# Kernel tuning notes

Hardware: AMD Instinct MI355X
Metric: run time of the kernel (lower is better)

The kernel has to match this reference:

```python
import jax, jax.numpy as jnp
import numpy as np

DIM = 1024
HEADS = 16
DHEAD = 64
INNER = HEADS * DHEAD
B, N = 1, 2048
ROPE_BASE = 10000.0
LN_EPS = 1e-5


def rope_tables(seq_len, d, dtype):
    # theta_i = 1 / base^(2i/d); emb = cat(freqs, freqs) -> cos/sin [N, d]
    theta = 1.0 / (ROPE_BASE ** (jnp.arange(0, d, 2, dtype=dtype) / d))
    pos = jnp.arange(seq_len, dtype=dtype)
    freqs = pos[:, None] * theta[None, :]          # [N, d/2]
    emb = jnp.concatenate([freqs, freqs], axis=-1)  # [N, d]
    return jnp.cos(emb), jnp.sin(emb)


def apply_rotary(x, cos, sin):
    # x: [B,H,N,D], cos/sin: [N,D]; interleaved rotation as in the torch code
    x1, x2 = x[..., ::2], x[..., 1::2]
    x_rot = jnp.stack([-x2, x1], axis=-1).reshape(x.shape)
    return x * cos + x_rot * sin


def setup_inputs() -> dict:
    key = jax.random.key(0)
    ks = jax.random.split(key, 6)
    x = jax.random.normal(ks[0], (B, N, DIM), dtype=jnp.float32)
    gamma = jnp.ones((DIM,), dtype=jnp.float32)
    Wq = jax.random.normal(ks[1], (DIM, INNER), dtype=jnp.float32) * 0.02
    Wkv = jax.random.normal(ks[2], (DIM, 2 * INNER), dtype=jnp.float32) * 0.02
    # near-identity per-head bilinear transform (torch inits toward identity)
    W_bilinear = jnp.eye(DHEAD, dtype=jnp.float32)[None] + \
        jax.random.normal(ks[3], (HEADS, DHEAD, DHEAD), dtype=jnp.float32) * 0.02
    Wo = jax.random.normal(ks[4], (INNER, DIM), dtype=jnp.float32) * 0.02
    return {"x": x, "gamma": gamma, "Wq": Wq, "Wkv": Wkv,
            "W_bilinear": W_bilinear, "Wo": Wo}


def reference(x, gamma, Wq, Wkv, W_bilinear, Wo):
    b, n, _ = x.shape
    # LayerNorm (beta = 0 buffer)
    mu = jnp.mean(x, axis=-1, keepdims=True)
    var = jnp.var(x, axis=-1, keepdims=True)
    xn = (x - mu) / jnp.sqrt(var + LN_EPS) * gamma

    q = xn @ Wq                                    # [B,N,INNER]
    kv = xn @ Wkv                                  # [B,N,2*INNER]
    k, v = jnp.split(kv, 2, axis=-1)

    def to_heads(t):
        return t.reshape(b, n, HEADS, DHEAD).transpose(0, 2, 1, 3)  # [B,H,N,D]

    q, k, v = map(to_heads, (q, k, v))

    cos, sin = rope_tables(n, DHEAD, x.dtype)
    q = apply_rotary(q, cos, sin) * (DHEAD ** -0.5)
    k = apply_rotary(k, cos, sin)

    # per-head bilinear transform of K
    kt = jnp.einsum('bhnd,hde->bhne', k, W_bilinear)
    sim = jnp.einsum('bhid,bhjd->bhij', q, kt)      # [B,H,N,N]
    attn = jax.nn.softmax(sim, axis=-1)
    out = jnp.einsum('bhij,bhjd->bhid', attn, v)    # [B,H,N,D]
    out = out.transpose(0, 2, 1, 3).reshape(b, n, INNER)
    return out @ Wo
```

## Files before the change

### kernel.cpp

```cpp
#include <hip/hip_runtime.h>
#include <hip/hip_bf16.h>


typedef unsigned short u16;
typedef __attribute__((ext_vector_type(4))) float f32x4;
typedef __attribute__((ext_vector_type(8))) __bf16 bf16x8;

struct alignas(8) US4 { u16 x, y, z, w; };

__device__ __forceinline__ u16 f2bf(float f) {
  union { float f; unsigned u; } v; v.f = f;
  unsigned r = v.u + 0x7FFFu + ((v.u >> 16) & 1u);
  return (u16)(r >> 16);
}
__device__ __forceinline__ unsigned pk2bf(float a, float b) {
  float2 f; f.x = a; f.y = b;
  __hip_bfloat162 h = __float22bfloat162_rn(f);
  union { __hip_bfloat162 h; unsigned u; } v; v.h = h;
  return v.u;
}

typedef void GVOID __attribute__((address_space(1)));
typedef void LVOID __attribute__((address_space(3)));

#if defined(__has_builtin)
#if __has_builtin(__builtin_amdgcn_global_load_lds)
#define HAS_GLD_LDS 1
#endif
#endif

__device__ __forceinline__ void gld16(const void* g, void* l) {
#ifdef HAS_GLD_LDS
  __builtin_amdgcn_global_load_lds((GVOID*)(void*)g, (LVOID*)l, 16, 0, 0);
#else
  struct alignas(16) U4 { unsigned a, b, c, d; };
  *(U4*)l = *(const U4*)g;
#endif
}

__device__ __forceinline__ f32x4 MFMA(bf16x8 a, bf16x8 b, f32x4 c) {
  return __builtin_amdgcn_mfma_f32_16x16x32_bf16(a, b, c, 0, 0, 0);
}

__device__ __forceinline__ int swz(int r, int q) {
  return r * 32 + ((q ^ ((r >> 1) & 3)) << 3);
}
__device__ __forceinline__ int swz_src_colb(int o) {
  const int r = o >> 6;
  return ((((o >> 4) & 3) ^ ((r >> 1) & 3)) << 4);
}
__device__ __forceinline__ int mswz4(int ee, int c) {
  return ee * 64 + ((c ^ (ee & 15)) << 2);
}
__device__ __forceinline__ int mswz1(int ee, int q) {
  return ee * 64 + ((((q >> 2) ^ (ee & 15)) << 2) | (q & 3));
}

__global__ __launch_bounds__(256) void prep_kernel(
    const float* __restrict__ x, const float* __restrict__ gamma,
    const float* __restrict__ Wq, const float* __restrict__ Wkv,
    const float* __restrict__ Wo, const float* __restrict__ Wb,
    u16* __restrict__ xn, u16* __restrict__ wqkvT, u16* __restrict__ woT,
    u16* __restrict__ wbT) {
  __shared__ __align__(16) float smem[64 * 65];
  const int bid = blockIdx.x, t = threadIdx.x;
  if (bid < 1040) {
    const float* src; u16* dst; int C, R, bx, by;
    if (bid < 256)      { src = Wq;  dst = wqkvT; R = 1024; C = 1024; bx = bid & 15; by = bid >> 4; }
    else if (bid < 768) { int i = bid - 256; src = Wkv; dst = wqkvT + 1024 * 1024; R = 1024; C = 2048; bx = i & 31; by = i >> 5; }
    else if (bid < 1024){ int i = bid - 768; src = Wo;  dst = woT; R = 1024; C = 1024; bx = i & 15; by = i >> 4; }
    else { int h = bid - 1024; src = Wb + (size_t)h * 4096; dst = wbT + (size_t)h * 4096; R = 64; C = 64; bx = 0; by = 0; }
    float (*tile)[65] = (float(*)[65])smem;
    const int c0 = bx * 64, r0 = by * 64;
    const int tx = t & 63, ty = t >> 6;
#pragma unroll
    for (int i = 0; i < 16; i++)
      tile[ty + i * 4][tx] = src[(size_t)(r0 + ty + i * 4) * C + c0 + tx];
    __syncthreads();
#pragma unroll
    for (int i = 0; i < 16; i++)
      dst[(size_t)(c0 + ty + i * 4) * R + r0 + tx] = f2bf(tile[tx][ty + i * 4]);
  } else {
    const int n = bid - 1040;
    const int w = t >> 6, lane = t & 63;
    const float4 v = *(const float4*)&x[(size_t)n * 1024 + t * 4];
    float s = v.x + v.y + v.z + v.w;
    float q = v.x * v.x + v.y * v.y + v.z * v.z + v.w * v.w;
#pragma unroll
    for (int off = 32; off; off >>= 1) {
      s += __shfl_down(s, off);
      q += __shfl_down(q, off);
    }
    if (lane == 0) { smem[w] = s; smem[4 + w] = q; }
    __syncthreads();
    s = smem[0] + smem[1] + smem[2] + smem[3];
    q = smem[4] + smem[5] + smem[6] + smem[7];
    const float mean = s * (1.0f / 1024.0f);
    const float var = q * (1.0f / 1024.0f) - mean * mean;
    const float inv = rsqrtf(var + 1e-5f);
    const float4 g = *(const float4*)&gamma[t * 4];
    US4 o;
    o.x = f2bf((v.x - mean) * inv * g.x);
    o.y = f2bf((v.y - mean) * inv * g.y);
    o.z = f2bf((v.z - mean) * inv * g.z);
    o.w = f2bf((v.w - mean) * inv * g.w);
    *(US4*)&xn[(size_t)n * 1024 + t * 4] = o;
  }
}

__global__ __launch_bounds__(256, 2) void gemm_qkv(
    const u16* __restrict__ A, const u16* __restrict__ B,
    const u16* __restrict__ wbT, u16* __restrict__ qh,
    u16* __restrict__ kth, u16* __restrict__ vt) {
  __shared__ u16 As[2 * 128 * 32];
  __shared__ u16 Bs[2 * 128 * 32];
  __shared__ u16 krs[2 * 8192];
  const int K = 1024;
  const int t = threadIdx.x;
  const int w = t >> 6, lane = t & 63, quad = lane >> 4, cc = lane & 15;
  const int bm = blockIdx.y << 7, bn = blockIdx.x << 7;
  const int wm = (w >> 1) << 6, wn = (w & 1) << 6;
  const f32x4 fzero = {0.f, 0.f, 0.f, 0.f};
  f32x4 acc[4][4];
#pragma unroll
  for (int i = 0; i < 4; i++)
#pragma unroll
    for (int j = 0; j < 4; j++) acc[i][j] = fzero;

  const char* gA = (const char*)A;
  const char* gB = (const char*)B;
  for (int k0 = 0; k0 < K; k0 += 64) {
    __syncthreads();
#pragma unroll
    for (int i = 0; i < 4; i++) {
      const int o = (i * 256 + t) * 16;
      const int sub = o >> 13, row = (o >> 6) & 127, colb = swz_src_colb(o);
      gld16(gA + (((size_t)(bm + row) * K + k0 + sub * 32) << 1) + colb, (char*)As + o);
      gld16(gB + (((size_t)(bn + row) * K + k0 + sub * 32) << 1) + colb, (char*)Bs + o);
    }
    __syncthreads();
#pragma unroll
    for (int ks = 0; ks < 2; ks++) {
      bf16x8 af[4], bfr[4];
#pragma unroll
      for (int mi = 0; mi < 4; mi++)
        af[mi] = *(const bf16x8*)&As[ks * 4096 + swz(wm + mi * 16 + cc, quad)];
#pragma unroll
      for (int ni = 0; ni < 4; ni++)
        bfr[ni] = *(const bf16x8*)&Bs[ks * 4096 + swz(wn + ni * 16 + cc, quad)];
#pragma unroll
      for (int mi = 0; mi < 4; mi++)
#pragma unroll
        for (int ni = 0; ni < 4; ni++)
          acc[mi][ni] = MFMA(af[mi], bfr[ni], acc[mi][ni]);
    }
  }

  const int region = blockIdx.x >> 3;
  if (region == 0) {
#pragma unroll
    for (int ni = 0; ni < 4; ni++) {
      const int col = bn + wn + ni * 16 + cc;
      const int h = (col >> 6) & 15, d = col & 63;
      const float theta = __expf(-(float)(col & 31) * 0.2878231366242557f);
      const float sgn = (col & 1) ? 1.0f : -1.0f;
#pragma unroll
      for (int mi = 0; mi < 4; mi++) {
        const int row0 = bm + wm + mi * 16 + quad * 4;
#pragma unroll
        for (int r = 0; r < 4; r++) {
          const float val = acc[mi][ni][r];
          const float pr = __shfl_xor(val, 1);
          float sv, cv;
          __sincosf(theta * (float)(row0 + r), &sv, &cv);
          qh[((size_t)h * 2048 + row0 + r) * 64 + d] =
              f2bf((val * cv + sgn * pr * sv) * 0.125f);
        }
      }
    }
  } else if (region == 2) {
#pragma unroll
    for (int ni = 0; ni < 4; ni++) {
      const int col = bn + wn + ni * 16 + cc;
      const int h = (col >> 6) & 15, d = col & 63;
      u16* base = vt + ((size_t)h * 64 + d) * 2048;
#pragma unroll
      for (int mi = 0; mi < 4; mi++) {
        const int row0 = bm + wm + mi * 16 + quad * 4;
        uint2 pk;
        pk.x = pk2bf(acc[mi][ni][0], acc[mi][ni][1]);
        pk.y = pk2bf(acc[mi][ni][2], acc[mi][ni][3]);
        *(uint2*)&base[row0] = pk;
      }
    }
  } else {
    const int h2 = w & 1;
    u16* krh = krs + h2 * 8192;
#pragma unroll
    for (int ni = 0; ni < 4; ni++) {
      const int dloc = ni * 16 + cc;
      const int dsub = dloc >> 5;
      const int chunk = (dloc & 31) >> 3, elem = dloc & 7;
      const int col = bn + wn + ni * 16 + cc;
      const float theta = __expf(-(float)(col & 31) * 0.2878231366242557f);
      const float sgn = (col & 1) ? 1.0f : -1.0f;
#pragma unroll
      for (int mi = 0; mi < 4; mi++) {
        const int lrow0 = wm + mi * 16 + quad * 4;
#pragma unroll
        for (int r = 0; r < 4; r++) {
          const float val = acc[mi][ni][r];
          const float pr = __shfl_xor(val, 1);
          float sv, cv;
          __sincosf(theta * (float)(bm + lrow0 + r), &sv, &cv);
          const int row = lrow0 + r;
          krh[dsub * 4096 + row * 32 + ((chunk ^ ((row >> 1) & 3)) << 3) + elem] =
              f2bf(val * cv + sgn * pr * sv);
        }
      }
    }
    __syncthreads();
    const int hg0 = (bn >> 6) & 15;
#pragma unroll
    for (int i = 0; i < 2; i++) {
      const int o = (i * 256 + t) * 16;
      const int row = o >> 6;
      const int dsub = row >> 6, e = row & 63;
      const int colb = swz_src_colb(o);
      gld16((const char*)wbT + (((size_t)hg0 * 4096 + e * 64 + dsub * 32) << 1) + colb,
            (char*)As + o);
      gld16((const char*)wbT + (((size_t)(hg0 + 1) * 4096 + e * 64 + dsub * 32) << 1) + colb,
            (char*)Bs + o);
    }
    __syncthreads();
    const int wmrow = (w >> 1) << 6;
    const u16* Bsel = h2 ? Bs : As;
    f32x4 acc2[4][4];
#pragma unroll
    for (int i = 0; i < 4; i++)
#pragma unroll
      for (int j = 0; j < 4; j++) acc2[i][j] = fzero;
#pragma unroll
    for (int dsub = 0; dsub < 2; dsub++) {
      bf16x8 bfr[4];
#pragma unroll
      for (int et = 0; et < 4; et++)
        bfr[et] = *(const bf16x8*)&Bsel[swz(dsub * 64 + et * 16 + cc, quad)];
#pragma unroll
      for (int mi = 0; mi < 4; mi++) {
        const bf16x8 af = *(const bf16x8*)&krh[dsub * 4096 + swz(wmrow + mi * 16 + cc, quad)];
#pragma unroll
        for (int et = 0; et < 4; et++)
          acc2[mi][et] = MFMA(af, bfr[et], acc2[mi][et]);
      }
    }
    u16* Ck = kth + (size_t)(hg0 + h2) * 2048 * 64;
#pragma unroll
    for (int mi = 0; mi < 4; mi++) {
      const int n0 = bm + wmrow + mi * 16 + quad * 4;
#pragma unroll
      for (int et = 0; et < 4; et++) {
        const int e = et * 16 + cc;
#pragma unroll
        for (int r = 0; r < 4; r++)
          Ck[(size_t)(n0 + r) * 64 + e] = f2bf(acc2[mi][et][r]);
      }
    }
  }
}

__global__ __launch_bounds__(256, 2) void attn_kernel(
    const u16* __restrict__ qh, const u16* __restrict__ kth,
    const u16* __restrict__ vt, u16* __restrict__ aout) {
  __shared__ u16 Ks[2 * 128 * 32];
  __shared__ u16 Vs[4 * 64 * 32];
  __shared__ u16 Ps[4 * 64 * 32];
  const int t = threadIdx.x;
  const int w = t >> 6, lane = t & 63, quad = lane >> 4, cc = lane & 15;
  const int bid = blockIdx.x;
  const int h = (bid & 7) + ((bid >> 8) << 3);
  const int q0 = ((bid >> 3) & 31) << 6;
  const size_t hq = (size_t)h * (2048 * 64);
  const f32x4 fzero = {0.f, 0.f, 0.f, 0.f};
  const int g4 = (cc >> 1) & 3;

  bf16x8 ones;
  {
    union { u16 u; __bf16 b; } one; one.u = 0x3F80;
#pragma unroll
    for (int i = 0; i < 8; i++) ones[i] = one.b;
  }

#pragma unroll
  for (int i = 0; i < 2; i++) {
    const int o = (i * 256 + t) * 16;
    const int sub = o >> 12, row = (o >> 6) & 63, colb = swz_src_colb(o);
    gld16((const char*)qh + ((hq + (size_t)(q0 + row) * 64 + sub * 32) << 1) + colb,
          (char*)Ks + o);
  }
  __syncthreads();
  bf16x8 qf[4][2];
#pragma unroll
  for (int qn = 0; qn < 4; qn++)
#pragma unroll
    for (int ds = 0; ds < 2; ds++)
      qf[qn][ds] = *(const bf16x8*)&Ks[swz(ds * 64 + qn * 16 + cc, quad)];

  f32x4 oacc[4][4];
  f32x4 lacc[4];
#pragma unroll
  for (int mi = 0; mi < 4; mi++) {
    lacc[mi] = fzero;
#pragma unroll
    for (int et = 0; et < 4; et++) oacc[mi][et] = fzero;
  }

  u16* const psw = Ps + (w << 11);

  for (int jt = 0; jt < 16; jt++) {
    const int j0 = jt << 7;
    __syncthreads();
#pragma unroll
    for (int i = 0; i < 4; i++) {
      const int o = (i * 256 + t) * 16;
      const int colb = swz_src_colb(o);
      const int sub = o >> 13, row = (o >> 6) & 127;
      gld16((const char*)kth + ((hq + (size_t)(j0 + row) * 64 + sub * 32) << 1) + colb,
            (char*)Ks + o);
      const int vsub = o >> 12, vrow = (o >> 6) & 63;
      gld16((const char*)vt + ((hq + (size_t)vrow * 2048 + j0 + vsub * 32) << 1) + colb,
            (char*)Vs + o);
    }
    __syncthreads();

#pragma unroll
    for (int jm = 0; jm < 2; jm++) {
      const bf16x8 kf0 = *(const bf16x8*)&Ks[swz(w * 32 + jm * 16 + cc, quad)];
      const bf16x8 kf1 = *(const bf16x8*)&Ks[swz(128 + w * 32 + jm * 16 + cc, quad)];
      const int c16 = ((jm << 1) + (quad >> 1)) ^ g4;
      const int coff = (c16 << 3) + ((quad & 1) << 2);
#pragma unroll
      for (int qn = 0; qn < 4; qn++) {
        f32x4 s = MFMA(kf0, qf[qn][0], fzero);
        s = MFMA(kf1, qf[qn][1], s);
        uint2 pk;
        pk.x = pk2bf(__expf(s[0]), __expf(s[1]));
        pk.y = pk2bf(__expf(s[2]), __expf(s[3]));
        *(uint2*)&psw[((qn * 16 + cc) << 5) + coff] = pk;
      }
    }

    bf16x8 vf[4];
#pragma unroll
    for (int et = 0; et < 4; et++)
      vf[et] = *(const bf16x8*)&Vs[swz(w * 64 + et * 16 + cc, quad)];
#pragma unroll
    for (int mi = 0; mi < 4; mi++) {
      const bf16x8 pa = *(const bf16x8*)&psw[swz(mi * 16 + cc, quad)];
      lacc[mi] = MFMA(pa, ones, lacc[mi]);
#pragma unroll
      for (int et = 0; et < 4; et++) oacc[mi][et] = MFMA(pa, vf[et], oacc[mi][et]);
    }
  }

  float* OA = (float*)Ks;
  float* OB = (float*)Vs;
  float* lP = (float*)Ps;
  __syncthreads();
  if (w >= 2) {
    float* dst = (w == 2) ? OA : OB;
#pragma unroll
    for (int mi = 0; mi < 4; mi++) {
#pragma unroll
      for (int et = 0; et < 4; et++) {
        const int ee = et * 16 + cc;
        *(f32x4*)&dst[mswz4(ee, mi * 4 + quad)] = oacc[mi][et];
      }
      if (cc == 0)
#pragma unroll
        for (int r = 0; r < 4; r++)
          lP[64 * w + mi * 16 + quad * 4 + r] = lacc[mi][r];
    }
  }
  __syncthreads();
  if (w < 2) {
    const float* src = (w == 0) ? OA : OB;
    const float* lsrc = &lP[64 * (w + 2)];
#pragma unroll
    for (int mi = 0; mi < 4; mi++) {
#pragma unroll
      for (int et = 0; et < 4; et++) {
        const int ee = et * 16 + cc;
        oacc[mi][et] += *(const f32x4*)&src[mswz4(ee, mi * 4 + quad)];
      }
#pragma unroll
      for (int r = 0; r < 4; r++)
        lacc[mi][r] += lsrc[mi * 16 + quad * 4 + r];
    }
  }
  __syncthreads();
  if (w < 2) {
    float* dst = (w == 0) ? OA : OB;
#pragma unroll
    for (int mi = 0; mi < 4; mi++) {
#pragma unroll
      for (int et = 0; et < 4; et++) {
        const int ee = et * 16 + cc;
        *(f32x4*)&dst[mswz4(ee, mi * 4 + quad)] = oacc[mi][et];
      }
      if (cc == 0)
#pragma unroll
        for (int r = 0; r < 4; r++)
          lP[64 * w + mi * 16 + quad * 4 + r] = lacc[mi][r];
    }
  }
  __syncthreads();
  {
    const int q = lane;
    const float linv = 1.0f / (lP[q] + lP[64 + q]);
    unsigned obuf[8];
#pragma unroll
    for (int e = 0; e < 8; e++) {
      const int e0 = w * 16 + e * 2, e1 = e0 + 1;
      obuf[e] = pk2bf((OA[mswz1(e0, q)] + OB[mswz1(e0, q)]) * linv,
                      (OA[mswz1(e1, q)] + OB[mswz1(e1, q)]) * linv);
    }
    uint4* dst = (uint4*)&aout[(size_t)(q0 + q) * 1024 + h * 64 + w * 16];
    dst[0] = *(uint4*)&obuf[0];
    dst[1] = *(uint4*)&obuf[4];
  }
}

__global__ __launch_bounds__(256, 2) void gemm64_bt_f32(
    const u16* __restrict__ A, const u16* __restrict__ B, float* __restrict__ C,
    int M, int N, int K) {
  __shared__ u16 As[2 * 64 * 32];
  __shared__ u16 Bs[2 * 64 * 32];
  const int t = threadIdx.x;
  const int w = t >> 6, lane = t & 63, quad = lane >> 4, cc = lane & 15;
  const int bm = blockIdx.y << 6, bn = blockIdx.x << 6;
  const int wm = (w >> 1) << 5, wn = (w & 1) << 5;
  const f32x4 fzero = {0.f, 0.f, 0.f, 0.f};
  f32x4 acc[2][2];
#pragma unroll
  for (int i = 0; i < 2; i++)
#pragma unroll
    for (int j = 0; j < 2; j++) acc[i][j] = fzero;

  const char* gA = (const char*)A;
  const char* gB = (const char*)B;
  for (int k0 = 0; k0 < K; k0 += 64) {
    __syncthreads();
#pragma unroll
    for (int i = 0; i < 2; i++) {
      const int o = (i * 256 + t) * 16;
      const int sub = o >> 12, row = (o >> 6) & 63, colb = swz_src_colb(o);
      gld16(gA + (((size_t)(bm + row) * K + k0 + sub * 32) << 1) + colb, (char*)As + o);
      gld16(gB + (((size_t)(bn + row) * K + k0 + sub * 32) << 1) + colb, (char*)Bs + o);
    }
    __syncthreads();
#pragma unroll
    for (int ks = 0; ks < 2; ks++) {
      bf16x8 af[2], bfr[2];
#pragma unroll
      for (int mi = 0; mi < 2; mi++)
        af[mi] = *(const bf16x8*)&As[ks * 2048 + swz(wm + mi * 16 + cc, quad)];
#pragma unroll
      for (int ni = 0; ni < 2; ni++)
        bfr[ni] = *(const bf16x8*)&Bs[ks * 2048 + swz(wn + ni * 16 + cc, quad)];
#pragma unroll
      for (int mi = 0; mi < 2; mi++)
#pragma unroll
        for (int ni = 0; ni < 2; ni++)
          acc[mi][ni] = MFMA(af[mi], bfr[ni], acc[mi][ni]);
    }
  }
#pragma unroll
  for (int mi = 0; mi < 2; mi++) {
    const int row = bm + wm + mi * 16 + quad * 4;
#pragma unroll
    for (int ni = 0; ni < 2; ni++) {
      const int col = bn + wn + ni * 16 + cc;
#pragma unroll
      for (int r = 0; r < 4; r++) C[(size_t)(row + r) * N + col] = acc[mi][ni][r];
    }
  }
}

extern "C" void kernel_launch(void* const* d_in, const int* in_sizes, int n_in,
                              void* d_out, int out_size, void* d_ws, size_t ws_size,
                              hipStream_t stream) {
  (void)in_sizes; (void)n_in; (void)out_size; (void)ws_size;
  const float* x     = (const float*)d_in[0];
  const float* gamma = (const float*)d_in[1];
  const float* Wq    = (const float*)d_in[2];
  const float* Wkv   = (const float*)d_in[3];
  const float* Wb    = (const float*)d_in[4];
  const float* Wo    = (const float*)d_in[5];
  float* out = (float*)d_out;
  char* ws = (char*)d_ws;

  const size_t OFF_XN    = 0;
  const size_t OFF_WQKVT = 4194304;
  const size_t OFF_WOT   = 10485760;
  const size_t OFF_WBT   = 12582912;
  const size_t OFF_QH    = 12713984;
  const size_t OFF_KTH   = 16908288;
  const size_t OFF_VT    = 21102592;
  const size_t OFF_AOUT  = 25296896;

  u16* xn    = (u16*)(ws + OFF_XN);
  u16* wqkvT = (u16*)(ws + OFF_WQKVT);
  u16* woT   = (u16*)(ws + OFF_WOT);
  u16* wbT   = (u16*)(ws + OFF_WBT);
  u16* qh    = (u16*)(ws + OFF_QH);
  u16* kth   = (u16*)(ws + OFF_KTH);
  u16* vt    = (u16*)(ws + OFF_VT);
  u16* aout  = (u16*)(ws + OFF_AOUT);

  prep_kernel<<<3088, 256, 0, stream>>>(x, gamma, Wq, Wkv, Wo, Wb,
                                        xn, wqkvT, woT, wbT);
  gemm_qkv<<<dim3(24, 16), 256, 0, stream>>>(xn, wqkvT, wbT, qh, kth, vt);
  attn_kernel<<<512, 256, 0, stream>>>(qh, kth, vt, aout);
  gemm64_bt_f32<<<dim3(16, 32), 256, 0, stream>>>(aout, woT, out, 2048, 1024, 1024);
}
```

Baseline: 148.3 us.

## Double-buffer K/V tiles in attention kernel to overlap loads with compute

The attention kernel's shared memory becomes one pool holding two K and two V buffers, which allows double buffering. The next K/V tile is issued before the current tile's QK, exp and PV MFMAs run, and the loop is unrolled by two so each iteration needs only one barrier instead of two. The Q tile is staged through the P buffer and the epilogue reuses the K/V buffers. This aims to hide global-to-LDS latency, at the cost of raising LDS per block from 48 KB to 80 KB, which could limit occupancy under the two-blocks-per-CU launch bound.

```diff
diff --git a/kernel.cpp b/kernel.cpp
--- a/kernel.cpp
+++ b/kernel.cpp
@@ -272,9 +272,12 @@
 __global__ __launch_bounds__(256, 2) void attn_kernel(
     const u16* __restrict__ qh, const u16* __restrict__ kth,
     const u16* __restrict__ vt, u16* __restrict__ aout) {
-  __shared__ u16 Ks[2 * 128 * 32];
-  __shared__ u16 Vs[4 * 64 * 32];
-  __shared__ u16 Ps[4 * 64 * 32];
+  __shared__ __align__(16) u16 lds[40960];
+  u16* const Kb0 = lds;
+  u16* const Kb1 = lds + 8192;
+  u16* const Vb0 = lds + 16384;
+  u16* const Vb1 = lds + 24576;
+  u16* const Ps  = lds + 32768;
   const int t = threadIdx.x;
   const int w = t >> 6, lane = t & 63, quad = lane >> 4, cc = lane & 15;
   const int bid = blockIdx.x;
@@ -291,21 +294,7 @@
     for (int i = 0; i < 8; i++) ones[i] = one.b;
   }
 
-#pragma unroll
-  for (int i = 0; i < 2; i++) {
-    const int o = (i * 256 + t) * 16;
-    const int sub = o >> 12, row = (o >> 6) & 63, colb = swz_src_colb(o);
-    gld16((const char*)qh + ((hq + (size_t)(q0 + row) * 64 + sub * 32) << 1) + colb,
-          (char*)Ks + o);
-  }
-  __syncthreads();
   bf16x8 qf[4][2];
-#pragma unroll
-  for (int qn = 0; qn < 4; qn++)
-#pragma unroll
-    for (int ds = 0; ds < 2; ds++)
-      qf[qn][ds] = *(const bf16x8*)&Ks[swz(ds * 64 + qn * 16 + cc, quad)];
-
   f32x4 oacc[4][4];
   f32x4 lacc[4];
 #pragma unroll
@@ -317,26 +306,26 @@
 
   u16* const psw = Ps + (w << 11);
 
-  for (int jt = 0; jt < 16; jt++) {
-    const int j0 = jt << 7;
-    __syncthreads();
+  auto PREFETCH = [&](int jtn, u16* KD, u16* VD) {
+    const int j0n = jtn << 7;
 #pragma unroll
     for (int i = 0; i < 4; i++) {
       const int o = (i * 256 + t) * 16;
       const int colb = swz_src_colb(o);
       const int sub = o >> 13, row = (o >> 6) & 127;
-      gld16((const char*)kth + ((hq + (size_t)(j0 + row) * 64 + sub * 32) << 1) + colb,
-            (char*)Ks + o);
+      gld16((const char*)kth + ((hq + (size_t)(j0n + row) * 64 + sub * 32) << 1) + colb,
+            (char*)KD + o);
       const int vsub = o >> 12, vrow = (o >> 6) & 63;
-      gld16((const char*)vt + ((hq + (size_t)vrow * 2048 + j0 + vsub * 32) << 1) + colb,
-            (char*)Vs + o);
-    }
-    __syncthreads();
-
+      gld16((const char*)vt + ((hq + (size_t)vrow * 2048 + j0n + vsub * 32) << 1) + colb,
+            (char*)VD + o);
+    }
+  };
+
+  auto COMPUTE = [&](const u16* KS, const u16* VS) {
 #pragma unroll
     for (int jm = 0; jm < 2; jm++) {
-      const bf16x8 kf0 = *(const bf16x8*)&Ks[swz(w * 32 + jm * 16 + cc, quad)];
-      const bf16x8 kf1 = *(const bf16x8*)&Ks[swz(128 + w * 32 + jm * 16 + cc, quad)];
+      const bf16x8 kf0 = *(const bf16x8*)&KS[swz(w * 32 + jm * 16 + cc, quad)];
+      const bf16x8 kf1 = *(const bf16x8*)&KS[swz(128 + w * 32 + jm * 16 + cc, quad)];
       const int c16 = ((jm << 1) + (quad >> 1)) ^ g4;
       const int coff = (c16 << 3) + ((quad & 1) << 2);
 #pragma unroll
@@ -349,11 +338,10 @@
         *(uint2*)&psw[((qn * 16 + cc) << 5) + coff] = pk;
       }
     }
-
     bf16x8 vf[4];
 #pragma unroll
     for (int et = 0; et < 4; et++)
-      vf[et] = *(const bf16x8*)&Vs[swz(w * 64 + et * 16 + cc, quad)];
+      vf[et] = *(const bf16x8*)&VS[swz(w * 64 + et * 16 + cc, quad)];
 #pragma unroll
     for (int mi = 0; mi < 4; mi++) {
       const bf16x8 pa = *(const bf16x8*)&psw[swz(mi * 16 + cc, quad)];
@@ -361,12 +349,36 @@
 #pragma unroll
       for (int et = 0; et < 4; et++) oacc[mi][et] = MFMA(pa, vf[et], oacc[mi][et]);
     }
-  }
-
-  float* OA = (float*)Ks;
-  float* OB = (float*)Vs;
-  float* lP = (float*)Ps;
+  };
+
+#pragma unroll
+  for (int i = 0; i < 2; i++) {
+    const int o = (i * 256 + t) * 16;
+    const int sub = o >> 12, row = (o >> 6) & 63, colb = swz_src_colb(o);
+    gld16((const char*)qh + ((hq + (size_t)(q0 + row) * 64 + sub * 32) << 1) + colb,
+          (char*)Ps + o);
+  }
+  PREFETCH(0, Kb0, Vb0);
   __syncthreads();
+#pragma unroll
+  for (int qn = 0; qn < 4; qn++)
+#pragma unroll
+    for (int ds = 0; ds < 2; ds++)
+      qf[qn][ds] = *(const bf16x8*)&Ps[swz(ds * 64 + qn * 16 + cc, quad)];
+  __syncthreads();
+
+  for (int jt = 0; jt < 16; jt += 2) {
+    PREFETCH(jt + 1, Kb1, Vb1);
+    COMPUTE(Kb0, Vb0);
+    __syncthreads();
+    if (jt + 2 < 16) PREFETCH(jt + 2, Kb0, Vb0);
+    COMPUTE(Kb1, Vb1);
+    __syncthreads();
+  }
+
+  float* OA = (float*)Kb0;
+  float* OB = (float*)Kb1;
+  float* lP = (float*)Vb0;
   if (w >= 2) {
     float* dst = (w == 2) ? OA : OB;
 #pragma unroll
```

Result: no change. 146.6 us (-1.1%).
